# Performance work log

Measured on AMD Instinct MI355X. Metric: run time of the kernel, lower is better.

The kernel has to match this reference:

```python
import jax, jax.numpy as jnp
import numpy as np

NUM_BANKS = 32  # bank size (num_heads in __init__)
D_HEAD = 128
D_MODEL = 2048
B, S, K = 2, 1024, 4  # batch, seq, selected heads per token


def setup_inputs() -> dict:
    key = jax.random.key(0)
    k1, k2, k3, k4, k5 = jax.random.split(key, 5)
    tensor = jax.random.normal(k1, (B, S, K, D_HEAD), dtype=jnp.float32)
    head_selection = jax.random.randint(k2, (B, S, K), 0, NUM_BANKS)
    head_probabilities = jax.random.uniform(k3, (B, S, K), dtype=jnp.float32)
    # Banked linear parameters: one (d_head, d_model) matrix + bias per bank.
    W = jax.random.normal(k4, (NUM_BANKS, D_HEAD, D_MODEL), dtype=jnp.float32) * (1.0 / np.sqrt(D_HEAD))
    b = jax.random.normal(k5, (NUM_BANKS, D_MODEL), dtype=jnp.float32) * 0.01
    return {"tensor": tensor, "head_selection": head_selection,
            "head_probabilities": head_probabilities, "W": W, "b": b}


def reference(tensor, head_selection, head_probabilities, W, b):
    # BankedLinear: per (token, head-slot) select weight matrix W[sel] and
    # compute x @ W[sel] + b[sel] -> (..., k, d_model).
    # Implemented as a one-hot dispatch so the contraction is a single
    # grouped-GEMM-shaped einsum instead of materializing an
    # (B,S,K,d_head,d_model) gathered weight tensor.
    onehot = jax.nn.one_hot(head_selection, NUM_BANKS, dtype=tensor.dtype)  # (B,S,K,N)
    proj = jnp.einsum('bskd,bskn,ndm->bskm', tensor, onehot, W)             # (B,S,K,d_model)
    proj = proj + jnp.einsum('bskn,nm->bskm', onehot, b)                    # gathered bias
    # Head merge: matmul(proj^T, probs.unsqueeze(-1)).squeeze(-1)
    # == probability-weighted sum over the head dimension.
    out = jnp.einsum('bskm,bsk->bsm', proj, head_probabilities)             # (B,S,d_model)
    return out
```

## Files before the change

kernel.cpp:

```cpp
#include <hip/hip_runtime.h>
#include <hip/hip_bf16.h>

#define NBANK 32
#define DHEAD 128
#define DMODEL 2048
#define NSLOT 8192
#define NTOK 2048

typedef __attribute__((ext_vector_type(8))) short short8;
typedef __attribute__((ext_vector_type(8))) float float8;
typedef __attribute__((ext_vector_type(4))) float f32x4;

__device__ __forceinline__ unsigned short f2bf(float f) {
    union { __hip_bfloat16 h; unsigned short u; } cvt;
    cvt.h = __float2bfloat16(f);
    return cvt.u;
}
__device__ __forceinline__ float bf2f(unsigned short u) {
    union { float f; unsigned int v; } cvt;
    cvt.v = ((unsigned int)u) << 16;
    return cvt.f;
}

__global__ void convW_kernel(const float* __restrict__ W,
                             unsigned short* __restrict__ wfrag) {
    int t = blockIdx.x * 256 + threadIdx.x;
    int lane = t & 63;
    int kk = (t >> 6) & 3;
    int mt = (t >> 8) & 127;
    int bank = t >> 15;
    int m = mt * 16 + (lane & 15);
    int kbase = kk * 32 + (lane >> 4) * 8;
    const float* src = W + ((size_t)bank * DHEAD + kbase) * DMODEL + m;
    short8 o;
    #pragma unroll
    for (int v = 0; v < 8; ++v)
        o[v] = (short)f2bf(src[v * DMODEL]);
    reinterpret_cast<short8*>(wfrag)[t] = o;
}

__global__ void bucket_kernel(const int* __restrict__ sel,
                              int* __restrict__ counts,
                              int* __restrict__ lists) {
    __shared__ int lcount[NBANK];
    __shared__ int lbase[NBANK];
    int tid = threadIdx.x;
    int slot = blockIdx.x * 256 + tid;
    if (tid < NBANK) lcount[tid] = 0;
    __syncthreads();
    int bank = sel[slot];
    int mypos = atomicAdd(&lcount[bank], 1);
    __syncthreads();
    if (tid < NBANK) lbase[tid] = atomicAdd(&counts[tid], lcount[tid]);
    __syncthreads();
    lists[bank * NSLOT + lbase[bank] + mypos] = slot;
}

__global__ __launch_bounds__(256, 4)
void gemm_kernel(const unsigned short* __restrict__ wfrag,
                 const float* __restrict__ x,
                 const int* __restrict__ counts,
                 const int* __restrict__ lists,
                 const float* __restrict__ probs,
                 unsigned short* __restrict__ proj) {
    __shared__ __align__(16) unsigned short A_lds[16 * DHEAD];
    __shared__ int slots_lds[16];

    int tid = threadIdx.x;
    int w = tid >> 6;
    int lane = tid & 63;
    int lane_lo = lane & 15;
    int lane_hi = lane >> 4;
    int bank = blockIdx.y;
    int mw = blockIdx.x * 128 + w * 32;
    int mt0 = mw >> 4;
    int cnt = counts[bank];

    const short8* wf = reinterpret_cast<const short8*>(wfrag);
    short8 bw[4][2];
    #pragma unroll
    for (int nf = 0; nf < 2; ++nf)
        #pragma unroll
        for (int kk = 0; kk < 4; ++kk)
            bw[kk][nf] = wf[((((bank * 128 + mt0 + nf) * 4) + kk) << 6) + lane];

    for (int rt = blockIdx.z; rt * 16 < cnt; rt += gridDim.z) {
        __syncthreads();
        {
            int row = tid >> 4, chunk = tid & 15;
            int ridx = rt * 16 + row;
            int slot = (ridx < cnt) ? lists[bank * NSLOT + ridx] : -1;
            if (chunk == 0) slots_lds[row] = slot;
            short8 a = {0, 0, 0, 0, 0, 0, 0, 0};
            if (slot >= 0) {
                float p = probs[slot];
                float8 xv = reinterpret_cast<const float8*>(x + (size_t)slot * DHEAD)[chunk];
                #pragma unroll
                for (int j = 0; j < 8; ++j)
                    a[j] = (short)f2bf(xv[j] * p);
            }
            int byteoff = row * 256 + ((chunk * 16) ^ ((row & 7) << 4));
            *reinterpret_cast<short8*>(reinterpret_cast<char*>(A_lds) + byteoff) = a;
        }
        __syncthreads();

        f32x4 acc0 = {0.f, 0.f, 0.f, 0.f};
        f32x4 acc1 = {0.f, 0.f, 0.f, 0.f};
        #pragma unroll
        for (int kk = 0; kk < 4; ++kk) {
            int row = lane_lo;
            int byteoff = row * 256 + ((kk * 64 + lane_hi * 16) ^ ((row & 7) << 4));
            short8 a = *reinterpret_cast<const short8*>(
                reinterpret_cast<char*>(A_lds) + byteoff);
            acc0 = __builtin_amdgcn_mfma_f32_16x16x32_bf16(a, bw[kk][0], acc0, 0, 0, 0);
            acc1 = __builtin_amdgcn_mfma_f32_16x16x32_bf16(a, bw[kk][1], acc1, 0, 0, 0);
        }

        #pragma unroll
        for (int v = 0; v < 4; ++v) {
            int row = lane_hi * 4 + v;
            int slot = slots_lds[row];
            if (slot >= 0) {
                unsigned short* pr = proj + (size_t)slot * DMODEL + mw;
                pr[lane_lo]      = f2bf(acc0[v]);
                pr[16 + lane_lo] = f2bf(acc1[v]);
            }
        }
    }
}

__global__ void merge_kernel(const unsigned short* __restrict__ proj,
                             const int* __restrict__ sel,
                             const float* __restrict__ probs,
                             const float* __restrict__ bias,
                             float* __restrict__ out) {
    int tid = threadIdx.x;
    int tok = blockIdx.x;
    float8 acc = {0.f, 0.f, 0.f, 0.f, 0.f, 0.f, 0.f, 0.f};
    #pragma unroll
    for (int k = 0; k < 4; ++k) {
        int slot = tok * 4 + k;
        short8 pr = reinterpret_cast<const short8*>(proj + (size_t)slot * DMODEL)[tid];
        float p = probs[slot];
        int bk = sel[slot];
        float8 bv = reinterpret_cast<const float8*>(bias + (size_t)bk * DMODEL)[tid];
        #pragma unroll
        for (int j = 0; j < 8; ++j)
            acc[j] += bf2f((unsigned short)pr[j]) + p * bv[j];
    }
    reinterpret_cast<float8*>(out + (size_t)tok * DMODEL)[tid] = acc;
}

extern "C" void kernel_launch(void* const* d_in, const int* in_sizes, int n_in,
                              void* d_out, int out_size, void* d_ws, size_t ws_size,
                              hipStream_t stream) {
    const float* x     = (const float*)d_in[0];
    const int*   sel   = (const int*)  d_in[1];
    const float* probs = (const float*)d_in[2];
    const float* W     = (const float*)d_in[3];
    const float* bias  = (const float*)d_in[4];
    float* out = (float*)d_out;

    char* ws = (char*)d_ws;
    int* counts = (int*)ws;
    int* lists  = (int*)(ws + 1024);
    unsigned short* wfrag = (unsigned short*)(ws + (2u << 20));
    unsigned short* proj  = (unsigned short*)(ws + (19u << 20));

    hipMemsetAsync(counts, 0, 128, stream);
    convW_kernel<<<4096, 256, 0, stream>>>(W, wfrag);
    bucket_kernel<<<32, 256, 0, stream>>>(sel, counts, lists);
    gemm_kernel<<<dim3(16, 32, 4), 256, 0, stream>>>(wfrag, x, counts, lists,
                                                     probs, proj);
    merge_kernel<<<2048, 256, 0, stream>>>(proj, sel, probs, bias, out);
}
```

Before: 128.3 us.

## Pre-compact scaled bf16 activations per bank and stream them into LDS directly

Adds a compact_kernel that gathers each bank's selected rows, scales them by the head probability, converts them to bf16 and stores them contiguously per bank. The GEMM then fills LDS with __builtin_amdgcn_global_load_lds, skipping the per-tile gather and conversion in registers. Each wave now covers 64 output columns instead of 32, which halves the x-dimension of the grid. This costs an extra kernel launch and an intermediate buffer, and it assumes no bank gets more than 1024 rows.

```diff
diff --git a/kernel.cpp b/kernel.cpp
--- a/kernel.cpp
+++ b/kernel.cpp
@@ -6,6 +6,7 @@
 #define DMODEL 2048
 #define NSLOT 8192
 #define NTOK 2048
+#define XCROWS 1024
 
 typedef __attribute__((ext_vector_type(8))) short short8;
 typedef __attribute__((ext_vector_type(8))) float float8;
@@ -56,12 +57,31 @@
     lists[bank * NSLOT + lbase[bank] + mypos] = slot;
 }
 
+__global__ void compact_kernel(const float* __restrict__ x,
+                               const float* __restrict__ probs,
+                               const int* __restrict__ counts,
+                               const int* __restrict__ lists,
+                               unsigned short* __restrict__ xc) {
+    int bank = blockIdx.x;
+    int wv = (threadIdx.x >> 6) + blockIdx.y * 4;
+    int lane = threadIdx.x & 63;
+    int cnt = counts[bank];
+    for (int pos = wv; pos < cnt; pos += 16) {
+        int slot = lists[bank * NSLOT + pos];
+        float p = probs[slot];
+        float2 v = reinterpret_cast<const float2*>(x + (size_t)slot * DHEAD)[lane];
+        ushort2 o;
+        o.x = f2bf(v.x * p);
+        o.y = f2bf(v.y * p);
+        reinterpret_cast<ushort2*>(xc + ((size_t)bank * XCROWS + pos) * DHEAD)[lane] = o;
+    }
+}
+
 __global__ __launch_bounds__(256, 4)
 void gemm_kernel(const unsigned short* __restrict__ wfrag,
-                 const float* __restrict__ x,
+                 const unsigned short* __restrict__ xc,
                  const int* __restrict__ counts,
                  const int* __restrict__ lists,
-                 const float* __restrict__ probs,
                  unsigned short* __restrict__ proj) {
     __shared__ __align__(16) unsigned short A_lds[16 * DHEAD];
     __shared__ int slots_lds[16];
@@ -72,48 +92,47 @@
     int lane_lo = lane & 15;
     int lane_hi = lane >> 4;
     int bank = blockIdx.y;
-    int mw = blockIdx.x * 128 + w * 32;
+    int mw = blockIdx.x * 256 + w * 64;
     int mt0 = mw >> 4;
     int cnt = counts[bank];
 
     const short8* wf = reinterpret_cast<const short8*>(wfrag);
-    short8 bw[4][2];
+    short8 bw[4][4];
     #pragma unroll
-    for (int nf = 0; nf < 2; ++nf)
+    for (int nf = 0; nf < 4; ++nf)
         #pragma unroll
         for (int kk = 0; kk < 4; ++kk)
             bw[kk][nf] = wf[((((bank * 128 + mt0 + nf) * 4) + kk) << 6) + lane];
 
-    for (int rt = blockIdx.z; rt * 16 < cnt; rt += gridDim.z) {
+    int row16 = tid >> 4, j = tid & 15;
+    const char* xc_b = reinterpret_cast<const char*>(xc)
+                     + ((size_t)bank * XCROWS + row16) * 256
+                     + ((j ^ (row16 & 7)) << 4);
+    char* lds_b = reinterpret_cast<char*>(A_lds);
+    char* lds_dst = lds_b + (w << 10);
+
+    for (int rt = blockIdx.z; rt * 16 < cnt; rt += 4) {
         __syncthreads();
-        {
-            int row = tid >> 4, chunk = tid & 15;
-            int ridx = rt * 16 + row;
-            int slot = (ridx < cnt) ? lists[bank * NSLOT + ridx] : -1;
-            if (chunk == 0) slots_lds[row] = slot;
-            short8 a = {0, 0, 0, 0, 0, 0, 0, 0};
-            if (slot >= 0) {
-                float p = probs[slot];
-                float8 xv = reinterpret_cast<const float8*>(x + (size_t)slot * DHEAD)[chunk];
-                #pragma unroll
-                for (int j = 0; j < 8; ++j)
-                    a[j] = (short)f2bf(xv[j] * p);
-            }
-            int byteoff = row * 256 + ((chunk * 16) ^ ((row & 7) << 4));
-            *reinterpret_cast<short8*>(reinterpret_cast<char*>(A_lds) + byteoff) = a;
+        __builtin_amdgcn_global_load_lds(
+            (const __attribute__((address_space(1))) void*)(xc_b + (size_t)rt * 16 * 256),
+            (__attribute__((address_space(3))) void*)lds_dst, 16, 0, 0);
+        if (tid < 16) {
+            int ridx = rt * 16 + tid;
+            slots_lds[tid] = (ridx < cnt) ? lists[bank * NSLOT + ridx] : -1;
         }
         __syncthreads();
 
-        f32x4 acc0 = {0.f, 0.f, 0.f, 0.f};
-        f32x4 acc1 = {0.f, 0.f, 0.f, 0.f};
+        f32x4 acc[4] = {{0.f,0.f,0.f,0.f},{0.f,0.f,0.f,0.f},
+                        {0.f,0.f,0.f,0.f},{0.f,0.f,0.f,0.f}};
         #pragma unroll
         for (int kk = 0; kk < 4; ++kk) {
-            int row = lane_lo;
-            int byteoff = row * 256 + ((kk * 64 + lane_hi * 16) ^ ((row & 7) << 4));
-            short8 a = *reinterpret_cast<const short8*>(
-                reinterpret_cast<char*>(A_lds) + byteoff);
-            acc0 = __builtin_amdgcn_mfma_f32_16x16x32_bf16(a, bw[kk][0], acc0, 0, 0, 0);
-            acc1 = __builtin_amdgcn_mfma_f32_16x16x32_bf16(a, bw[kk][1], acc1, 0, 0, 0);
+            int byteoff = lane_lo * 256 +
+                          ((kk * 64 + lane_hi * 16) ^ ((lane_lo & 7) << 4));
+            short8 a = *reinterpret_cast<const short8*>(lds_b + byteoff);
+            #pragma unroll
+            for (int nf = 0; nf < 4; ++nf)
+                acc[nf] = __builtin_amdgcn_mfma_f32_16x16x32_bf16(
+                              a, bw[kk][nf], acc[nf], 0, 0, 0);
         }
 
         #pragma unroll
@@ -121,9 +140,10 @@
             int row = lane_hi * 4 + v;
             int slot = slots_lds[row];
             if (slot >= 0) {
-                unsigned short* pr = proj + (size_t)slot * DMODEL + mw;
-                pr[lane_lo]      = f2bf(acc0[v]);
-                pr[16 + lane_lo] = f2bf(acc1[v]);
+                unsigned short* pr = proj + (size_t)slot * DMODEL + mw + lane_lo;
+                #pragma unroll
+                for (int nf = 0; nf < 4; ++nf)
+                    pr[nf * 16] = f2bf(acc[nf][v]);
             }
         }
     }
@@ -145,8 +165,8 @@
         int bk = sel[slot];
         float8 bv = reinterpret_cast<const float8*>(bias + (size_t)bk * DMODEL)[tid];
         #pragma unroll
-        for (int j = 0; j < 8; ++j)
-            acc[j] += bf2f((unsigned short)pr[j]) + p * bv[j];
+        for (int jj = 0; jj < 8; ++jj)
+            acc[jj] += bf2f((unsigned short)pr[jj]) + p * bv[jj];
     }
     reinterpret_cast<float8*>(out + (size_t)tok * DMODEL)[tid] = acc;
 }
@@ -164,13 +184,14 @@
     char* ws = (char*)d_ws;
     int* counts = (int*)ws;
     int* lists  = (int*)(ws + 1024);
-    unsigned short* wfrag = (unsigned short*)(ws + (2u << 20));
-    unsigned short* proj  = (unsigned short*)(ws + (19u << 20));
+    unsigned short* xc    = (unsigned short*)(ws + (2u  << 20));
+    unsigned short* wfrag = (unsigned short*)(ws + (12u << 20));
+    unsigned short* proj  = (unsigned short*)(ws + (32u << 20));
 
     hipMemsetAsync(counts, 0, 128, stream);
     convW_kernel<<<4096, 256, 0, stream>>>(W, wfrag);
     bucket_kernel<<<32, 256, 0, stream>>>(sel, counts, lists);
-    gemm_kernel<<<dim3(16, 32, 4), 256, 0, stream>>>(wfrag, x, counts, lists,
-                                                     probs, proj);
+    compact_kernel<<<dim3(32, 4), 256, 0, stream>>>(x, probs, counts, lists, xc);
+    gemm_kernel<<<dim3(8, 32, 4), 256, 0, stream>>>(wfrag, xc, counts, lists, proj);
     merge_kernel<<<2048, 256, 0, stream>>>(proj, sel, probs, bias, out);
 }
```

Result: slower. 132.6 us (+3.4%).
